# Kernel tuning notes

Hardware: AMD Instinct MI355X
Metric: run time of the kernel (lower is better)

Reference implementation:

```python
import jax, jax.numpy as jnp
import numpy as np

B, C, H, W = 8, 256, 128, 128
HEADS = 4
HEAD_DIM = C // HEADS  # 64
SCALE = HEAD_DIM ** -0.5


def setup_inputs() -> dict:
    key = jax.random.key(0)
    k1, k2, k3 = jax.random.split(key, 3)
    x = jax.random.normal(k1, (B, C, H, W), dtype=jnp.float32)
    # 1x1 convs == per-pixel linear layers; kaiming-ish small init
    Wqkv = jax.random.normal(k2, (3 * C, C), dtype=jnp.float32) * (1.0 / np.sqrt(C))
    bqkv = jnp.zeros((3 * C,), dtype=jnp.float32)
    Wproj = jax.random.normal(k3, (C, C), dtype=jnp.float32) * (1.0 / np.sqrt(C))
    bproj = jnp.zeros((C,), dtype=jnp.float32)
    return {"x": x, "Wqkv": Wqkv, "bqkv": bqkv, "Wproj": Wproj, "bproj": bproj}


def reference(x, Wqkv, bqkv, Wproj, bproj):
    b, c, h, w = x.shape
    hw = h * w
    xf = x.reshape(b, c, hw)  # [b, c, hw]
    # 1x1 conv QKV projection
    qkv = jnp.einsum('bcn,oc->bon', xf, Wqkv) + bqkv[None, :, None]  # [b, 3c, hw]
    qkv = qkv.reshape(b, 3, HEADS, HEAD_DIM, hw)
    q, k, v = qkv[:, 0], qkv[:, 1], qkv[:, 2]  # each [b, heads, d, hw]
    # channel attention: [b, heads, d, d]
    attn = jnp.einsum('bhdn,bhen->bhde', q, k) * SCALE
    attn = jax.nn.softmax(attn, axis=-1)
    out = jnp.einsum('bhde,bhen->bhdn', attn, v).reshape(b, c, hw)
    # output 1x1 conv
    out = jnp.einsum('bcn,oc->bon', out, Wproj) + bproj[None, :, None]
    return out.reshape(b, c, h, w)
```

## Files before the change

kernel.cpp:

```cpp
#include <hip/hip_runtime.h>
#include <hip/hip_bf16.h>
#include <stdint.h>


#define HW 16384
#define SCALE_F 0.125f
#define NF 16384.0f

typedef __attribute__((ext_vector_type(8))) short bf16x8;
typedef __attribute__((ext_vector_type(4))) float f32x4;

__device__ __forceinline__ unsigned short f2bf(float f) {
    union { float f; uint32_t u; } v; v.f = f;
    uint32_t u = v.u;
    return (unsigned short)((u + 0x7fffu + ((u >> 16) & 1u)) >> 16);
}
__device__ __forceinline__ float bf2f(unsigned short s) {
    union { uint32_t u; float f; } v; v.u = ((uint32_t)s) << 16;
    return v.f;
}

__global__ __launch_bounds__(512) void gram(
        const float* __restrict__ x, float* __restrict__ partG,
        float* __restrict__ parts_s) {
    const int kc = blockIdx.x;
    const int b  = blockIdx.y;
    __shared__ __align__(16) unsigned short Hs[2][256 * 32];
    __shared__ __align__(16) unsigned short Ls[2][256 * 32];
    const int tid = threadIdx.x, lane = tid & 63, w = tid >> 6;
    const int l15 = lane & 15, lg = lane >> 4;
    const int wr = w >> 1, wc = w & 1;
    const int srow = tid >> 1, shalf = tid & 1;
    const int m4 = (srow >> 1) & 3;
    const float* xb = x + (size_t)b * 256 * HW + (size_t)srow * HW + kc * 512 + shalf * 16;
    f32x4 acc[4][8] = {};
    float rs = 0.f;
    float4 ld0[4], ld1[4];

#define LOADR(dst, kstep)                                                       \
    {                                                                           \
        const float4* src = reinterpret_cast<const float4*>(xb + (kstep) * 32); \
        dst[0] = src[0]; dst[1] = src[1]; dst[2] = src[2]; dst[3] = src[3];     \
    }
#define STORE(sel, buf)                                                         \
    {                                                                           \
        _Pragma("unroll")                                                       \
        for (int cq = 0; cq < 2; ++cq) {                                        \
            union { unsigned short u[8]; uint4 v; } Hu, Lu;                     \
            const float vv[8] = {buf[2*cq].x, buf[2*cq].y, buf[2*cq].z, buf[2*cq].w, \
                                 buf[2*cq+1].x, buf[2*cq+1].y, buf[2*cq+1].z, buf[2*cq+1].w}; \
            _Pragma("unroll")                                                   \
            for (int i = 0; i < 8; ++i) {                                       \
                Hu.u[i] = f2bf(vv[i]);                                          \
                Lu.u[i] = f2bf(vv[i] - bf2f(Hu.u[i]));                          \
                rs += vv[i];                                                    \
            }                                                                   \
            const int slot = ((shalf * 2 + cq) ^ m4) << 4;                      \
            *reinterpret_cast<uint4*>((char*)(&Hs[sel][0]) + srow * 64 + slot) = Hu.v; \
            *reinterpret_cast<uint4*>((char*)(&Ls[sel][0]) + srow * 64 + slot) = Lu.v; \
        }                                                                       \
    }
#define DO_MFMA(sel)                                                            \
    {                                                                           \
        bf16x8 fah[4], fal[4];                                                  \
        _Pragma("unroll")                                                       \
        for (int i = 0; i < 4; ++i) {                                           \
            const int row = wr * 64 + i * 16 + l15;                             \
            const int off = row * 64 + ((lg ^ ((row >> 1) & 3)) << 4);          \
            fah[i] = *reinterpret_cast<const bf16x8*>((const char*)&Hs[sel][0] + off); \
            fal[i] = *reinterpret_cast<const bf16x8*>((const char*)&Ls[sel][0] + off); \
        }                                                                       \
        _Pragma("unroll")                                                       \
        for (int j = 0; j < 8; ++j) {                                           \
            const int row = wc * 128 + j * 16 + l15;                            \
            const int off = row * 64 + ((lg ^ ((row >> 1) & 3)) << 4);          \
            const bf16x8 fbh = *reinterpret_cast<const bf16x8*>((const char*)&Hs[sel][0] + off); \
            const bf16x8 fbl = *reinterpret_cast<const bf16x8*>((const char*)&Ls[sel][0] + off); \
            _Pragma("unroll")                                                   \
            for (int i = 0; i < 4; ++i) {                                       \
                acc[i][j] = __builtin_amdgcn_mfma_f32_16x16x32_bf16(fah[i], fbh, acc[i][j], 0, 0, 0); \
                acc[i][j] = __builtin_amdgcn_mfma_f32_16x16x32_bf16(fah[i], fbl, acc[i][j], 0, 0, 0); \
                acc[i][j] = __builtin_amdgcn_mfma_f32_16x16x32_bf16(fal[i], fbh, acc[i][j], 0, 0, 0); \
            }                                                                   \
        }                                                                       \
    }

    LOADR(ld0, 0);
    LOADR(ld1, 1);
    STORE(0, ld0);
    __syncthreads();
    for (int t = 0; t < 16; ++t) {
        if (t < 14) {
            if (t & 1) { LOADR(ld1, t + 2); } else { LOADR(ld0, t + 2); }
        }
        DO_MFMA(t & 1);
        if (t < 15) {
            if ((t + 1) & 1) { STORE((t + 1) & 1, ld1); } else { STORE((t + 1) & 1, ld0); }
        }
        __syncthreads();
    }
#undef LOADR
#undef STORE
#undef DO_MFMA

    rs += __shfl_xor(rs, 1);
    if ((tid & 1) == 0) parts_s[(size_t)(b * 32 + kc) * 256 + srow] = rs;

    float* pw = partG + (size_t)(b * 32 + kc) * 65536;
    #pragma unroll
    for (int i = 0; i < 4; ++i)
        #pragma unroll
        for (int rr = 0; rr < 4; ++rr) {
            const int m = wr * 64 + i * 16 + lg * 4 + rr;
            #pragma unroll
            for (int j = 0; j < 8; ++j)
                pw[m * 256 + wc * 128 + j * 16 + l15] = acc[i][j][rr];
        }
}

__global__ __launch_bounds__(256) void greduce(
        const float4* __restrict__ partG4, float4* __restrict__ G4) {
    const int g = blockIdx.x * 256 + threadIdx.x;
    const int b = g >> 14, i4 = g & 16383;
    float4 a = make_float4(0.f, 0.f, 0.f, 0.f);
    #pragma unroll 8
    for (int kc = 0; kc < 32; ++kc) {
        const float4 v = partG4[(size_t)(b * 32 + kc) * 16384 + i4];
        a.x += v.x; a.y += v.y; a.z += v.z; a.w += v.w;
    }
    G4[g] = a;
}

__global__ __launch_bounds__(512) void tlogits(
        const float* __restrict__ G, const float* __restrict__ Wqkv,
        const float* __restrict__ bqkv, const float* __restrict__ parts_s,
        float* __restrict__ attn) {
    const int bh = blockIdx.x, b = bh >> 2, h = bh & 3;
    const int tid = threadIdx.x;
    __shared__ __align__(16) float SM[38528];
    float* R1 = SM;
    float* R2 = SM + 16896;
    float* WQ = SM + 33792;
    float* SB = SM + 38144;
    float* QS = SM + 38400;
    float* KS = SM + 38464;
    const float* Gb = G + (size_t)b * 65536;
    const float* Wq = Wqkv + (size_t)(h * 64) * 256;
    const float* Wk = Wqkv + (size_t)(256 + h * 64) * 256;

    if (tid < 256) {
        float a = 0.f;
        #pragma unroll
        for (int kc = 0; kc < 32; ++kc)
            a += parts_s[(size_t)(b * 32 + kc) * 256 + tid];
        SB[tid] = a;
    }
    {
        const int e = tid >> 3, cq = (tid & 7) * 32;
        #pragma unroll
        for (int q = 0; q < 8; ++q) {
            const float4 w4 = *reinterpret_cast<const float4*>(Wk + (size_t)e * 256 + cq + q * 4);
            R2[(cq + q * 4 + 0) * 66 + e] = w4.x;
            R2[(cq + q * 4 + 1) * 66 + e] = w4.y;
            R2[(cq + q * 4 + 2) * 66 + e] = w4.z;
            R2[(cq + q * 4 + 3) * 66 + e] = w4.w;
        }
    }
    __syncthreads();
    if (tid < 64) {
        float a = 0.f;
        for (int c = 0; c < 256; ++c) a += R2[c * 66 + tid] * SB[c];
        KS[tid] = a;
    }

    const int dq = tid >> 5, cb = tid & 31;
    float tacc[4][8] = {};
    float qacc = 0.f;
    for (int cc = 0; cc < 4; ++cc) {
        {
            const int r = tid >> 3, cq = (tid & 7) * 32;
            #pragma unroll
            for (int q = 0; q < 8; ++q)
                *reinterpret_cast<float4*>(&R1[r * 264 + cq + q * 4]) =
                    *reinterpret_cast<const float4*>(Gb + (size_t)(cc * 64 + r) * 256 + cq + q * 4);
        }
        {
            const int r = tid >> 3, c8 = (tid & 7) * 8;
            *reinterpret_cast<float4*>(&WQ[r * 68 + c8]) =
                *reinterpret_cast<const float4*>(Wq + (size_t)r * 256 + cc * 64 + c8);
            *reinterpret_cast<float4*>(&WQ[r * 68 + c8 + 4]) =
                *reinterpret_cast<const float4*>(Wq + (size_t)r * 256 + cc * 64 + c8 + 4);
        }
        __syncthreads();
        for (int c = 0; c < 64; ++c) {
            float wv[4];
            #pragma unroll
            for (int i = 0; i < 4; ++i) wv[i] = WQ[(dq * 4 + i) * 68 + c];
            #pragma unroll
            for (int jj = 0; jj < 8; ++jj) {
                const float gv = R1[c * 264 + cb + 32 * jj];
                #pragma unroll
                for (int i = 0; i < 4; ++i) tacc[i][jj] += wv[i] * gv;
            }
        }
        if (tid < 64) {
            float a = 0.f;
            for (int c = 0; c < 64; ++c) a += WQ[tid * 68 + c] * SB[cc * 64 + c];
            qacc += a;
        }
        __syncthreads();
    }
    if (tid < 64) QS[tid] = qacc;
    #pragma unroll
    for (int i = 0; i < 4; ++i)
        #pragma unroll
        for (int jj = 0; jj < 8; ++jj)
            R1[(dq * 4 + i) * 264 + cb + 32 * jj] = tacc[i][jj];
    __syncthreads();

    const int e2 = tid & 31;
    float lacc[4][2] = {};
    for (int c = 0; c < 256; ++c) {
        float tv[4];
        #pragma unroll
        for (int i = 0; i < 4; ++i) tv[i] = R1[(dq * 4 + i) * 264 + c];
        #pragma unroll
        for (int k = 0; k < 2; ++k) {
            const float wv = R2[c * 66 + e2 * 2 + k];
            #pragma unroll
            for (int i = 0; i < 4; ++i) lacc[i][k] += tv[i] * wv;
        }
    }
    float* lgs = WQ;
    const float* bq = bqkv + h * 64;
    const float* bk = bqkv + 256 + h * 64;
    #pragma unroll
    for (int i = 0; i < 4; ++i) {
        const int d = dq * 4 + i;
        #pragma unroll
        for (int k = 0; k < 2; ++k) {
            const int e = e2 * 2 + k;
            lgs[d * 65 + e] = SCALE_F * (lacc[i][k] + bq[d] * KS[e] + bk[e] * QS[d] + NF * bq[d] * bk[e]);
        }
    }
    __syncthreads();
    if (tid < 64) {
        float m = -1e30f;
        for (int e = 0; e < 64; ++e) m = fmaxf(m, lgs[tid * 65 + e]);
        float sum = 0.f;
        for (int e = 0; e < 64; ++e) {
            const float ex = __expf(lgs[tid * 65 + e] - m);
            sum += ex;
            lgs[tid * 65 + e] = ex;
        }
        const float inv = 1.f / sum;
        float* ar = attn + ((size_t)bh * 64 + tid) * 64;
        for (int e = 0; e < 64; ++e) ar[e] = lgs[tid * 65 + e] * inv;
    }
}

__global__ __launch_bounds__(256) void buildMP(
        const float* __restrict__ attn, const float* __restrict__ Wproj,
        const float* __restrict__ Wqkv, const float* __restrict__ bqkv,
        const float* __restrict__ bproj, unsigned short* __restrict__ P,
        float* __restrict__ cvec) {
    const int blk = blockIdx.x;
    const int b = blk >> 4, o0 = (blk & 15) * 16;
    const int tid = threadIdx.x;
    __shared__ __align__(16) float U[16512];
    __shared__ __align__(16) float WpL[16 * 258];
    __shared__ __align__(16) float ML[16 * 258];
    const int og = tid >> 6, cb = tid & 63;

    {
        const float* ab = attn + (size_t)b * 16384;
        #pragma unroll
        for (int q = 0; q < 16; ++q)
            *reinterpret_cast<float4*>(&U[tid * 64 + q * 4]) =
                *reinterpret_cast<const float4*>(ab + tid * 64 + q * 4);
    }
    {
        const int r = tid >> 4, cc = (tid & 15) * 16;
        #pragma unroll
        for (int q = 0; q < 4; ++q)
            *reinterpret_cast<float4*>(&WpL[r * 258 + cc + q * 4]) =
                *reinterpret_cast<const float4*>(Wproj + (size_t)(o0 + r) * 256 + cc + q * 4);
    }
    __syncthreads();

    float macc[4][4] = {};
    #pragma unroll
    for (int j = 0; j < 4; ++j)
        for (int d = 0; d < 64; ++d) {
            const float a = U[j * 4096 + d * 64 + cb];
            #pragma unroll
            for (int i = 0; i < 4; ++i)
                macc[i][j] += WpL[(og * 4 + i) * 258 + j * 64 + d] * a;
        }
    #pragma unroll
    for (int i = 0; i < 4; ++i)
        #pragma unroll
        for (int j = 0; j < 4; ++j)
            ML[(og * 4 + i) * 258 + j * 64 + cb] = macc[i][j];
    __syncthreads();

    if (tid < 16) {
        const int o = o0 + tid;
        float a = bproj[o];
        for (int he = 0; he < 256; ++he) a += ML[tid * 258 + he] * bqkv[512 + he];
        cvec[b * 256 + o] = a;
    }

    float pacc[4][4] = {};
    for (int ch = 0; ch < 4; ++ch) {
        {
            const int r = tid >> 2, cc = (tid & 3) * 64;
            #pragma unroll
            for (int q = 0; q < 16; ++q)
                *reinterpret_cast<float4*>(&U[r * 258 + cc + q * 4]) =
                    *reinterpret_cast<const float4*>(Wqkv + (size_t)(512 + ch * 64 + r) * 256 + cc + q * 4);
        }
        __syncthreads();
        for (int he = 0; he < 64; ++he) {
            float mw[4];
            #pragma unroll
            for (int i = 0; i < 4; ++i) mw[i] = ML[(og * 4 + i) * 258 + ch * 64 + he];
            #pragma unroll
            for (int j = 0; j < 4; ++j) {
                const float wv = U[he * 258 + j * 64 + cb];
                #pragma unroll
                for (int i = 0; i < 4; ++i) pacc[i][j] += mw[i] * wv;
            }
        }
        __syncthreads();
    }
    unsigned short* Pb = P + (size_t)b * 65536;
    #pragma unroll
    for (int i = 0; i < 4; ++i)
        #pragma unroll
        for (int j = 0; j < 4; ++j)
            Pb[(size_t)(o0 + og * 4 + i) * 256 + j * 64 + cb] = f2bf(pacc[i][j]);
}

__global__ __launch_bounds__(512) void out_gemm(
        const unsigned short* __restrict__ P, const float* __restrict__ x,
        const float* __restrict__ cvec, float* __restrict__ out) {
    const int n0 = blockIdx.x * 128;
    const int b  = blockIdx.y;
    __shared__ __align__(16) unsigned short Bs[8 * 128 * 32];
    const int tid = threadIdx.x, lane = tid & 63, w = tid >> 6;
    const int wr = w >> 1, wc = w & 1;
    const int l15 = lane & 15, lg = lane >> 4;
    const unsigned short* Pb = P + (size_t)b * 65536;

    {
        const int sn = tid & 127;
        const int sg = tid >> 7;
        const int wslot = ((sg ^ ((sn >> 1) & 3)) << 4);
        const float* xcol = x + (size_t)b * 256 * HW + n0 + sn;
        float bv[2][8];
        #pragma unroll
        for (int i = 0; i < 8; ++i)
            bv[0][i] = xcol[(size_t)(sg * 8 + i) * HW];
        #pragma unroll
        for (int s = 0; s < 8; ++s) {
            if (s < 7) {
                #pragma unroll
                for (int i = 0; i < 8; ++i)
                    bv[(s + 1) & 1][i] = xcol[(size_t)((s + 1) * 32 + sg * 8 + i) * HW];
            }
            union { unsigned short u[8]; uint4 v; } Bu;
            #pragma unroll
            for (int i = 0; i < 8; ++i) Bu.u[i] = f2bf(bv[s & 1][i]);
            *reinterpret_cast<uint4*>((char*)Bs + s * 8192 + sn * 64 + wslot) = Bu.v;
        }
    }
    __syncthreads();

    f32x4 acc[4][4] = {};
    const int m4r = (l15 >> 1) & 3;
    #pragma unroll
    for (int s = 0; s < 8; ++s) {
        bf16x8 fp[4];
        #pragma unroll
        for (int i = 0; i < 4; ++i)
            fp[i] = *reinterpret_cast<const bf16x8*>(
                Pb + (size_t)(wr * 64 + i * 16 + l15) * 256 + s * 32 + lg * 8);
        #pragma unroll
        for (int j = 0; j < 4; ++j) {
            const int row = wc * 64 + j * 16 + l15;
            const bf16x8 fx = *reinterpret_cast<const bf16x8*>(
                (const char*)Bs + s * 8192 + row * 64 + ((lg ^ m4r) << 4));
            #pragma unroll
            for (int i = 0; i < 4; ++i)
                acc[i][j] = __builtin_amdgcn_mfma_f32_16x16x32_bf16(fx, fp[i], acc[i][j], 0, 0, 0);
        }
    }

    float* ob = out + (size_t)b * 256 * HW;
    #pragma unroll
    for (int i = 0; i < 4; ++i) {
        const int m = wr * 64 + i * 16 + l15;
        const float bp = cvec[b * 256 + m];
        #pragma unroll
        for (int j = 0; j < 4; ++j) {
            const int n = n0 + wc * 64 + j * 16 + lg * 4;
            float4 o4;
            o4.x = acc[i][j][0] + bp;
            o4.y = acc[i][j][1] + bp;
            o4.z = acc[i][j][2] + bp;
            o4.w = acc[i][j][3] + bp;
            *reinterpret_cast<float4*>(ob + (size_t)m * HW + n) = o4;
        }
    }
}

extern "C" void kernel_launch(void* const* d_in, const int* in_sizes, int n_in,
                              void* d_out, int out_size, void* d_ws, size_t ws_size,
                              hipStream_t stream) {
    const float* x     = (const float*)d_in[0];
    const float* Wqkv  = (const float*)d_in[1];
    const float* bqkv  = (const float*)d_in[2];
    const float* Wproj = (const float*)d_in[3];
    const float* bproj = (const float*)d_in[4];
    float* out = (float*)d_out;

    char* ws = (char*)d_ws;
    float* partG   = (float*)(ws);
    float* G       = (float*)(ws + 67108864);
    float* attn    = (float*)(ws + 69206016);
    unsigned short* P = (unsigned short*)(ws + 69730304);
    float* cvec    = (float*)(ws + 70778880);
    float* parts_s = (float*)(ws + 70787072);

    gram    <<<dim3(32, 8),  512, 0, stream>>>(x, partG, parts_s);
    greduce <<<512,          256, 0, stream>>>((const float4*)partG, (float4*)G);
    tlogits <<<32,           512, 0, stream>>>(G, Wqkv, bqkv, parts_s, attn);
    buildMP <<<128,          256, 0, stream>>>(attn, Wproj, Wqkv, bqkv, bproj, P, cvec);
    out_gemm<<<dim3(128, 8), 512, 0, stream>>>(P, x, cvec, out);
}
```

Before: 214.3 us.

## Split gram and out_gemm tiles in half to double block counts

```diff
diff --git a/kernel.cpp b/kernel.cpp
--- a/kernel.cpp
+++ b/kernel.cpp
@@ -23,32 +23,33 @@
 __global__ __launch_bounds__(512) void gram(
         const float* __restrict__ x, float* __restrict__ partG,
         float* __restrict__ parts_s) {
-    const int kc = blockIdx.x;
-    const int b  = blockIdx.y;
+    const int mh = blockIdx.x;
+    const int kc = blockIdx.y;
+    const int b  = blockIdx.z;
     __shared__ __align__(16) unsigned short Hs[2][256 * 32];
     __shared__ __align__(16) unsigned short Ls[2][256 * 32];
     const int tid = threadIdx.x, lane = tid & 63, w = tid >> 6;
     const int l15 = lane & 15, lg = lane >> 4;
-    const int wr = w >> 1, wc = w & 1;
+    const int wr = w & 1, wc = w >> 1;
     const int srow = tid >> 1, shalf = tid & 1;
     const int m4 = (srow >> 1) & 3;
     const float* xb = x + (size_t)b * 256 * HW + (size_t)srow * HW + kc * 512 + shalf * 16;
-    f32x4 acc[4][8] = {};
+    f32x4 acc[4][4] = {};
     float rs = 0.f;
-    float4 ld0[4], ld1[4];
-
-#define LOADR(dst, kstep)                                                       \
+    float4 ld[4];
+
+#define LOADR(kstep)                                                            \
     {                                                                           \
         const float4* src = reinterpret_cast<const float4*>(xb + (kstep) * 32); \
-        dst[0] = src[0]; dst[1] = src[1]; dst[2] = src[2]; dst[3] = src[3];     \
-    }
-#define STORE(sel, buf)                                                         \
+        ld[0] = src[0]; ld[1] = src[1]; ld[2] = src[2]; ld[3] = src[3];         \
+    }
+#define STORE(sel)                                                              \
     {                                                                           \
         _Pragma("unroll")                                                       \
         for (int cq = 0; cq < 2; ++cq) {                                        \
             union { unsigned short u[8]; uint4 v; } Hu, Lu;                     \
-            const float vv[8] = {buf[2*cq].x, buf[2*cq].y, buf[2*cq].z, buf[2*cq].w, \
-                                 buf[2*cq+1].x, buf[2*cq+1].y, buf[2*cq+1].z, buf[2*cq+1].w}; \
+            const float vv[8] = {ld[2*cq].x, ld[2*cq].y, ld[2*cq].z, ld[2*cq].w,\
+                                 ld[2*cq+1].x, ld[2*cq+1].y, ld[2*cq+1].z, ld[2*cq+1].w}; \
             _Pragma("unroll")                                                   \
             for (int i = 0; i < 8; ++i) {                                       \
                 Hu.u[i] = f2bf(vv[i]);                                          \
@@ -65,14 +66,14 @@
         bf16x8 fah[4], fal[4];                                                  \
         _Pragma("unroll")                                                       \
         for (int i = 0; i < 4; ++i) {                                           \
-            const int row = wr * 64 + i * 16 + l15;                             \
+            const int row = mh * 128 + wr * 64 + i * 16 + l15;                  \
             const int off = row * 64 + ((lg ^ ((row >> 1) & 3)) << 4);          \
             fah[i] = *reinterpret_cast<const bf16x8*>((const char*)&Hs[sel][0] + off); \
             fal[i] = *reinterpret_cast<const bf16x8*>((const char*)&Ls[sel][0] + off); \
         }                                                                       \
         _Pragma("unroll")                                                       \
-        for (int j = 0; j < 8; ++j) {                                           \
-            const int row = wc * 128 + j * 16 + l15;                            \
+        for (int j = 0; j < 4; ++j) {                                           \
+            const int row = wc * 64 + j * 16 + l15;                             \
             const int off = row * 64 + ((lg ^ ((row >> 1) & 3)) << 4);          \
             const bf16x8 fbh = *reinterpret_cast<const bf16x8*>((const char*)&Hs[sel][0] + off); \
             const bf16x8 fbl = *reinterpret_cast<const bf16x8*>((const char*)&Ls[sel][0] + off); \
@@ -85,18 +86,13 @@
         }                                                                       \
     }
 
-    LOADR(ld0, 0);
-    LOADR(ld1, 1);
-    STORE(0, ld0);
+    LOADR(0);
+    STORE(0);
     __syncthreads();
     for (int t = 0; t < 16; ++t) {
-        if (t < 14) {
-            if (t & 1) { LOADR(ld1, t + 2); } else { LOADR(ld0, t + 2); }
-        }
+        if (t < 15) LOADR(t + 1);
         DO_MFMA(t & 1);
-        if (t < 15) {
-            if ((t + 1) & 1) { STORE((t + 1) & 1, ld1); } else { STORE((t + 1) & 1, ld0); }
-        }
+        if (t < 15) STORE((t + 1) & 1);
         __syncthreads();
     }
 #undef LOADR
@@ -104,17 +100,18 @@
 #undef DO_MFMA
 
     rs += __shfl_xor(rs, 1);
-    if ((tid & 1) == 0) parts_s[(size_t)(b * 32 + kc) * 256 + srow] = rs;
+    if (mh == 0 && (tid & 1) == 0)
+        parts_s[(size_t)(b * 32 + kc) * 256 + srow] = rs;
 
     float* pw = partG + (size_t)(b * 32 + kc) * 65536;
     #pragma unroll
     for (int i = 0; i < 4; ++i)
         #pragma unroll
         for (int rr = 0; rr < 4; ++rr) {
-            const int m = wr * 64 + i * 16 + lg * 4 + rr;
-            #pragma unroll
-            for (int j = 0; j < 8; ++j)
-                pw[m * 256 + wc * 128 + j * 16 + l15] = acc[i][j][rr];
+            const int m = mh * 128 + wr * 64 + i * 16 + lg * 4 + rr;
+            #pragma unroll
+            for (int j = 0; j < 4; ++j)
+                pw[m * 256 + wc * 64 + j * 16 + l15] = acc[i][j][rr];
         }
 }
 
@@ -345,40 +342,39 @@
 __global__ __launch_bounds__(512) void out_gemm(
         const unsigned short* __restrict__ P, const float* __restrict__ x,
         const float* __restrict__ cvec, float* __restrict__ out) {
-    const int n0 = blockIdx.x * 128;
+    const int n0 = blockIdx.x * 64;
     const int b  = blockIdx.y;
-    __shared__ __align__(16) unsigned short Bs[8 * 128 * 32];
+    __shared__ __align__(16) unsigned short Bs[8 * 64 * 32];
     const int tid = threadIdx.x, lane = tid & 63, w = tid >> 6;
     const int wr = w >> 1, wc = w & 1;
     const int l15 = lane & 15, lg = lane >> 4;
     const unsigned short* Pb = P + (size_t)b * 65536;
 
     {
-        const int sn = tid & 127;
-        const int sg = tid >> 7;
-        const int wslot = ((sg ^ ((sn >> 1) & 3)) << 4);
+        const int sn = tid & 63;
+        const int sg = tid >> 6;
+        const int wbyte = (((sg >> 1) ^ ((sn >> 1) & 3)) << 4) + (sg & 1) * 8;
         const float* xcol = x + (size_t)b * 256 * HW + n0 + sn;
-        float bv[2][8];
-        #pragma unroll
-        for (int i = 0; i < 8; ++i)
-            bv[0][i] = xcol[(size_t)(sg * 8 + i) * HW];
+        float bv[2][4];
+        #pragma unroll
+        for (int i = 0; i < 4; ++i)
+            bv[0][i] = xcol[(size_t)(sg * 4 + i) * HW];
         #pragma unroll
         for (int s = 0; s < 8; ++s) {
             if (s < 7) {
                 #pragma unroll
-                for (int i = 0; i < 8; ++i)
-                    bv[(s + 1) & 1][i] = xcol[(size_t)((s + 1) * 32 + sg * 8 + i) * HW];
+                for (int i = 0; i < 4; ++i)
+                    bv[(s + 1) & 1][i] = xcol[(size_t)((s + 1) * 32 + sg * 4 + i) * HW];
             }
-            union { unsigned short u[8]; uint4 v; } Bu;
-            #pragma unroll
-            for (int i = 0; i < 8; ++i) Bu.u[i] = f2bf(bv[s & 1][i]);
-            *reinterpret_cast<uint4*>((char*)Bs + s * 8192 + sn * 64 + wslot) = Bu.v;
-        }
-    }
-    __syncthreads();
-
-    f32x4 acc[4][4] = {};
-    const int m4r = (l15 >> 1) & 3;
+            union { unsigned short u[4]; uint2 v; } Bu;
+            #pragma unroll
+            for (int i = 0; i < 4; ++i) Bu.u[i] = f2bf(bv[s & 1][i]);
+            *reinterpret_cast<uint2*>((char*)Bs + s * 4096 + sn * 64 + wbyte) = Bu.v;
+        }
+    }
+    __syncthreads();
+
+    f32x4 acc[4][2] = {};
     #pragma unroll
     for (int s = 0; s < 8; ++s) {
         bf16x8 fp[4];
@@ -387,10 +383,10 @@
             fp[i] = *reinterpret_cast<const bf16x8*>(
                 Pb + (size_t)(wr * 64 + i * 16 + l15) * 256 + s * 32 + lg * 8);
         #pragma unroll
-        for (int j = 0; j < 4; ++j) {
-            const int row = wc * 64 + j * 16 + l15;
+        for (int j = 0; j < 2; ++j) {
+            const int row = wc * 32 + j * 16 + l15;
             const bf16x8 fx = *reinterpret_cast<const bf16x8*>(
-                (const char*)Bs + s * 8192 + row * 64 + ((lg ^ m4r) << 4));
+                (const char*)Bs + s * 4096 + row * 64 + ((lg ^ ((row >> 1) & 3)) << 4));
             #pragma unroll
             for (int i = 0; i < 4; ++i)
                 acc[i][j] = __builtin_amdgcn_mfma_f32_16x16x32_bf16(fx, fp[i], acc[i][j], 0, 0, 0);
@@ -403,8 +399,8 @@
         const int m = wr * 64 + i * 16 + l15;
         const float bp = cvec[b * 256 + m];
         #pragma unroll
-        for (int j = 0; j < 4; ++j) {
-            const int n = n0 + wc * 64 + j * 16 + lg * 4;
+        for (int j = 0; j < 2; ++j) {
+            const int n = n0 + wc * 32 + j * 16 + lg * 4;
             float4 o4;
             o4.x = acc[i][j][0] + bp;
             o4.y = acc[i][j][1] + bp;
@@ -433,9 +429,9 @@
     float* cvec    = (float*)(ws + 70778880);
     float* parts_s = (float*)(ws + 70787072);
 
-    gram    <<<dim3(32, 8),  512, 0, stream>>>(x, partG, parts_s);
-    greduce <<<512,          256, 0, stream>>>((const float4*)partG, (float4*)G);
-    tlogits <<<32,           512, 0, stream>>>(G, Wqkv, bqkv, parts_s, attn);
-    buildMP <<<128,          256, 0, stream>>>(attn, Wproj, Wqkv, bqkv, bproj, P, cvec);
-    out_gemm<<<dim3(128, 8), 512, 0, stream>>>(P, x, cvec, out);
-}
+    gram    <<<dim3(2, 32, 8), 512, 0, stream>>>(x, partG, parts_s);
+    greduce <<<512,            256, 0, stream>>>((const float4*)partG, (float4*)G);
+    tlogits <<<32,             512, 0, stream>>>(G, Wqkv, bqkv, parts_s, attn);
+    buildMP <<<128,            256, 0, stream>>>(attn, Wproj, Wqkv, bqkv, bproj, P, cvec);
+    out_gemm<<<dim3(256, 8),   512, 0, stream>>>(P, x, cvec, out);
+}
```

After: 250.5 us. 16.9% more time.
